# Kernel optimization log

Hardware: AMD Instinct MI355X
Metric: run time of the kernel (lower is better)

Reference implementation:

```python
import jax, jax.numpy as jnp
import numpy as np

DIM = 768
NUM_HEADS = 12
HEAD_DIM = DIM // NUM_HEADS


def setup_inputs() -> dict:
    key = jax.random.key(0)
    k0, k1, k2 = jax.random.split(key, 3)
    B, N = 8, 1024
    x = jax.random.normal(k0, (B, N, DIM), dtype=jnp.float32)
    w_qkv = jax.random.normal(k1, (DIM, 3 * DIM), dtype=jnp.float32) * (DIM ** -0.5)
    b_qkv = jnp.zeros((3 * DIM,), dtype=jnp.float32)
    w_proj = jax.random.normal(k2, (DIM, DIM), dtype=jnp.float32) * (DIM ** -0.5)
    b_proj = jnp.zeros((DIM,), dtype=jnp.float32)
    return {"x": x, "w_qkv": w_qkv, "b_qkv": b_qkv, "w_proj": w_proj, "b_proj": b_proj}


def reference(x, w_qkv, b_qkv, w_proj, b_proj):
    B, N, C = x.shape
    scale = HEAD_DIM ** -0.5
    qkv = x @ w_qkv + b_qkv                                  # [B, N, 3*C]
    qkv = qkv.reshape(B, N, 3, NUM_HEADS, HEAD_DIM).transpose(2, 0, 3, 1, 4)
    q, k, v = qkv[0], qkv[1], qkv[2]                          # each [B, H, N, hd]
    attn = jnp.einsum('bhqd,bhkd->bhqk', q, k) * scale        # [B, H, N, N]
    attn = jax.nn.softmax(attn, axis=-1)
    out = jnp.einsum('bhqk,bhkd->bhqd', attn, v)              # [B, H, N, hd]
    out = out.transpose(0, 2, 1, 3).reshape(B, N, C)
    return out @ w_proj + b_proj
```

## Files before the change

kernel.cpp:

```cpp
#include <hip/hip_runtime.h>
#include <cstdint>
#include <cmath>

#define B_ 8
#define S_ 1024
#define D_ 768
#define H_ 12
#define HD_ 64

typedef __bf16 bf16;
typedef __attribute__((ext_vector_type(8))) __bf16 bf16x8;
typedef __attribute__((ext_vector_type(4))) float floatx4;

typedef const __attribute__((address_space(1))) unsigned int* gas_ptr;
typedef __attribute__((address_space(3))) unsigned int* las_ptr;

__device__ __forceinline__ void async_ld16(const void* g, void* l) {
    gas_ptr gp = (gas_ptr)(uintptr_t)g;
    las_ptr lp = (las_ptr)(unsigned)(uintptr_t)l;
    __builtin_amdgcn_global_load_lds(gp, lp, 16, 0, 0);
}

__device__ __forceinline__ void transpose_dev(const float* __restrict__ in,
                                              bf16* __restrict__ out,
                                              int N, int K, int n0, int k0,
                                              bf16 (*tile)[66], int tid) {
#pragma unroll
    for (int r = 0; r < 4; r++) {
        int idx = r * 256 + tid;
        int row = idx >> 4;
        int c0  = (idx & 15) * 4;
        float4 v = *(const float4*)(in + (size_t)(k0 + row) * N + n0 + c0);
        tile[c0 + 0][row] = (bf16)v.x;
        tile[c0 + 1][row] = (bf16)v.y;
        tile[c0 + 2][row] = (bf16)v.z;
        tile[c0 + 3][row] = (bf16)v.w;
    }
    __syncthreads();
#pragma unroll
    for (int r = 0; r < 2; r++) {
        int idx = r * 256 + tid;
        int orow = idx >> 3;
        int kk   = (idx & 7) * 8;
        union { bf16x8 v; bf16 e[8]; } u;
#pragma unroll
        for (int j = 0; j < 8; j++) u.e[j] = tile[orow][kk + j];
        *(bf16x8*)(out + (size_t)(n0 + orow) * K + k0 + kk) = u.v;
    }
}

__global__ __launch_bounds__(256) void prep_all(
    const float* __restrict__ x, const float* __restrict__ w_qkv,
    const float* __restrict__ w_proj,
    bf16* __restrict__ xb, bf16* __restrict__ wqkvt, bf16* __restrict__ wprojt)
{
    __shared__ bf16 tile[64][66];
    const int blk = blockIdx.x, tid = threadIdx.x;
    if (blk < 6144) {
        int i = (blk * 256 + tid) * 4;
        float4 v = *(const float4*)(x + i);
        xb[i]     = (bf16)v.x;
        xb[i + 1] = (bf16)v.y;
        xb[i + 2] = (bf16)v.z;
        xb[i + 3] = (bf16)v.w;
    } else if (blk < 6576) {
        int t = blk - 6144;
        transpose_dev(w_qkv, wqkvt, 2304, 768, (t % 36) * 64, (t / 36) * 64, tile, tid);
    } else {
        int t = blk - 6576;
        transpose_dev(w_proj, wprojt, 768, 768, (t % 12) * 64, (t / 12) * 64, tile, tid);
    }
}

__global__ void transpose_v(const bf16* __restrict__ vbuf, bf16* __restrict__ vt) {
    __shared__ bf16 tile[64][66];
    const int tid = threadIdx.x;
    const int kt = blockIdx.x, h = blockIdx.y, b = blockIdx.z;
    const bf16* src = vbuf + ((size_t)b * S_ + (size_t)kt * 64) * D_ + h * 64;
#pragma unroll
    for (int r = 0; r < 2; r++) {
        int idx = r * 256 + tid;
        int kr = idx >> 3;
        int d0 = (idx & 7) * 8;
        bf16x8 v = *(const bf16x8*)(src + (size_t)kr * D_ + d0);
#pragma unroll
        for (int j = 0; j < 8; j++) {
            int p  = d0 + j;
            int dt = (p >> 2) + 16 * (p & 3);
            tile[dt][kr] = v[j];
        }
    }
    __syncthreads();
    bf16* dst = vt + ((size_t)(b * H_ + h) * 64) * 1024 + kt * 64;
#pragma unroll
    for (int r = 0; r < 2; r++) {
        int idx = r * 256 + tid;
        int dr = idx >> 3;
        int k0 = (idx & 7) * 8;
        union { bf16x8 v; bf16 e[8]; } u;
#pragma unroll
        for (int j = 0; j < 8; j++) {
            int kp  = k0 + j;
            int grp = kp & 32;
            int w32 = kp & 31;
            int gg  = w32 >> 3;
            int jj  = w32 & 7;
            int tk  = grp + ((jj < 4) ? (4 * gg + jj) : (16 + 4 * gg + jj - 4));
            u.e[j] = tile[dr][tk];
        }
        *(bf16x8*)(dst + (size_t)dr * 1024 + k0) = u.v;
    }
}

__global__ __launch_bounds__(256, 2) void gemm_qkv(
    const bf16* __restrict__ A, const bf16* __restrict__ Bt,
    const float* __restrict__ bias,
    bf16* __restrict__ qpack, bf16* __restrict__ kpack, bf16* __restrict__ vbuf)
{
    __shared__ __align__(16) bf16 As[128 * 32];
    __shared__ __align__(16) bf16 Bs[128 * 32];
    const int N = 2304, K = 768;

    const int tid  = threadIdx.x;
    const int lane = tid & 63;
    const int w    = tid >> 6;
    const int wm   = (w >> 1) * 64;
    const int wn   = (w & 1) * 64;
    const long m0  = (long)blockIdx.y * 128;
    const long n0  = (long)blockIdx.x * 128;
    const int c    = lane & 15;
    const int g    = lane >> 4;

    const floatx4 fzero = {0.f, 0.f, 0.f, 0.f};
    floatx4 acc[4][4];
#pragma unroll
    for (int i = 0; i < 4; i++)
#pragma unroll
        for (int j = 0; j < 4; j++) acc[i][j] = fzero;

    for (int k0 = 0; k0 < K; k0 += 32) {
        __syncthreads();
#pragma unroll
        for (int r = 0; r < 2; r++) {
            const int idx = r * 256 + tid;
            const int row = idx >> 2;
            const int kk  = (idx & 3) * 8;
            async_ld16(A  + (m0 + row) * (long)K + k0 + kk, (char*)As + idx * 16);
            async_ld16(Bt + (n0 + row) * (long)K + k0 + kk, (char*)Bs + idx * 16);
        }
        __syncthreads();

        bf16x8 af[4], bfr[4];
#pragma unroll
        for (int i = 0; i < 4; i++) {
            af[i]  = *(const bf16x8*)(As + (wm + i * 16 + c) * 32 + g * 8);
            bfr[i] = *(const bf16x8*)(Bs + (wn + i * 16 + c) * 32 + g * 8);
        }
#pragma unroll
        for (int i = 0; i < 4; i++)
#pragma unroll
            for (int j = 0; j < 4; j++)
                acc[i][j] = __builtin_amdgcn_mfma_f32_16x16x32_bf16(af[i], bfr[j], acc[i][j], 0, 0, 0);
    }

    const int head = (int)((n0 + wn) >> 6);
    const int rm   = wm + g * 4;
    float bv[4];
#pragma unroll
    for (int j = 0; j < 4; j++) bv[j] = bias[(int)n0 + wn + c + 16 * j];
    const int bb    = (int)(m0 >> 10);
    const int sbase = ((int)m0 & 1023) + rm;

    if (head < 24) {
        const float sc = (head < 12) ? 0.125f : 1.0f;
        bf16* dst = ((head < 12) ? qpack : kpack)
                  + (((size_t)((bb * H_ + (head < 12 ? head : head - 12)) * 1024 + sbase)) << 6)
                  + 4 * c;
#pragma unroll
        for (int i = 0; i < 4; i++)
#pragma unroll
            for (int e = 0; e < 4; e++) {
                union { bf16 h4[4]; uint64_t u; } pk;
#pragma unroll
                for (int j = 0; j < 4; j++) pk.h4[j] = (bf16)((acc[i][j][e] + bv[j]) * sc);
                *(uint64_t*)(dst + (size_t)(i * 16 + e) * 64) = pk.u;
            }
    } else {
        bf16* dst = vbuf + ((size_t)(bb * 1024 + sbase)) * 768 + (head - 24) * 64 + 4 * c;
#pragma unroll
        for (int i = 0; i < 4; i++)
#pragma unroll
            for (int e = 0; e < 4; e++) {
                union { bf16 h4[4]; uint64_t u; } pk;
#pragma unroll
                for (int j = 0; j < 4; j++) pk.h4[j] = (bf16)(acc[i][j][e] + bv[j]);
                *(uint64_t*)(dst + (size_t)(i * 16 + e) * 768) = pk.u;
            }
    }
}

__global__ __launch_bounds__(256, 2) void gemm_bt(
    const bf16* __restrict__ A, const bf16* __restrict__ Bt,
    const float* __restrict__ bias, float* __restrict__ C,
    int M, int N, int K)
{
    __shared__ __align__(16) bf16 As[128 * 32];
    __shared__ __align__(16) bf16 Bs[128 * 32];

    const int tid  = threadIdx.x;
    const int lane = tid & 63;
    const int w    = tid >> 6;
    const int wm   = (w >> 1) * 64;
    const int wn   = (w & 1) * 64;
    const long m0  = (long)blockIdx.y * 128;
    const long n0  = (long)blockIdx.x * 128;
    const int c    = lane & 15;
    const int g    = lane >> 4;

    const floatx4 fzero = {0.f, 0.f, 0.f, 0.f};
    floatx4 acc[4][4];
#pragma unroll
    for (int i = 0; i < 4; i++)
#pragma unroll
        for (int j = 0; j < 4; j++) acc[i][j] = fzero;

    for (int k0 = 0; k0 < K; k0 += 32) {
        __syncthreads();
#pragma unroll
        for (int r = 0; r < 2; r++) {
            const int idx = r * 256 + tid;
            const int row = idx >> 2;
            const int kk  = (idx & 3) * 8;
            async_ld16(A  + (m0 + row) * (long)K + k0 + kk, (char*)As + idx * 16);
            async_ld16(Bt + (n0 + row) * (long)K + k0 + kk, (char*)Bs + idx * 16);
        }
        __syncthreads();

        bf16x8 af[4], bfr[4];
#pragma unroll
        for (int i = 0; i < 4; i++) {
            af[i]  = *(const bf16x8*)(As + (wm + i * 16 + c) * 32 + g * 8);
            bfr[i] = *(const bf16x8*)(Bs + (wn + i * 16 + c) * 32 + g * 8);
        }
#pragma unroll
        for (int i = 0; i < 4; i++)
#pragma unroll
            for (int j = 0; j < 4; j++)
                acc[i][j] = __builtin_amdgcn_mfma_f32_16x16x32_bf16(af[i], bfr[j], acc[i][j], 0, 0, 0);
    }

    const int cn = wn + c;
    const int rm = wm + g * 4;
#pragma unroll
    for (int j = 0; j < 4; j++) {
        const long gn = n0 + cn + j * 16;
        const float bv = bias[gn];
#pragma unroll
        for (int i = 0; i < 4; i++) {
            const long gm = m0 + rm + i * 16;
#pragma unroll
            for (int e = 0; e < 4; e++)
                C[(gm + e) * (long)N + gn] = acc[i][j][e] + bv;
        }
    }
}

__global__ __launch_bounds__(128, 3) void attn_fused(
    const bf16* __restrict__ qpack, const bf16* __restrict__ kpack,
    const bf16* __restrict__ vt, bf16* __restrict__ outp)
{
    __shared__ __align__(16) bf16 Ks[2048];
    __shared__ __align__(16) bf16 Vs[2048];

    const int tid  = threadIdx.x;
    const int lane = tid & 63;
    const int w    = tid >> 6;
    const int g    = lane >> 4;
    const int c    = lane & 15;

    const int id = blockIdx.x;
    const int bh = id % 96;
    const int qt = id / 96;
    const int h  = bh >> 3;
    const int b  = bh & 7;
    const int q0 = qt * 128 + w * 64;
    const bf16* qpb = qpack + ((size_t)(b * H_ + h) * 1024) * 64;
    const bf16* kpb = kpack + ((size_t)(b * H_ + h) * 1024) * 64;
    const bf16* vtb = vt    + ((size_t)(b * H_ + h) * 64) * 1024;

    bf16x8 qf[4][2];
#pragma unroll
    for (int qb = 0; qb < 4; qb++)
#pragma unroll
        for (int dc = 0; dc < 2; dc++)
            qf[qb][dc] = *(const bf16x8*)(qpb + (size_t)(q0 + qb * 16 + c) * 64 + dc * 32 + g * 8);

    union { uint32_t u[4]; bf16x8 v; } onesu;
    onesu.u[0] = onesu.u[1] = onesu.u[2] = onesu.u[3] = 0x3F803F80u;
    const bf16x8 onesf = onesu.v;

    const floatx4 fzero = {0.f, 0.f, 0.f, 0.f};
    floatx4 oacc[4][4];
    floatx4 lacc[4];
#pragma unroll
    for (int qb = 0; qb < 4; qb++) {
        lacc[qb] = fzero;
#pragma unroll
        for (int db = 0; db < 4; db++) oacc[qb][db] = fzero;
    }

    for (int kt = 0; kt < 32; kt++) {
        const int kg = kt * 32;
        __syncthreads();
#pragma unroll
        for (int r = 0; r < 2; r++) {
            const int i  = r * 128 + tid;
            const int dc = i >> 7, key = (i >> 2) & 31, dch = i & 3;
            async_ld16(kpb + (size_t)(kg + key) * 64 + dc * 32 + dch * 8, (char*)Ks + i * 16);
        }
#pragma unroll
        for (int r = 0; r < 2; r++) {
            const int i = r * 128 + tid;
            const int d = i >> 2, kch = i & 3;
            async_ld16(vtb + (size_t)d * 1024 + kg + kch * 8, (char*)Vs + i * 16);
        }
        __syncthreads();

        bf16x8 kf[2][2];
#pragma unroll
        for (int kb = 0; kb < 2; kb++)
#pragma unroll
            for (int dc = 0; dc < 2; dc++)
                kf[kb][dc] = *(const bf16x8*)(Ks + (dc * 32 + kb * 16 + c) * 32 + g * 8);

        bf16x8 vf[4];
#pragma unroll
        for (int db = 0; db < 4; db++)
            vf[db] = *(const bf16x8*)(Vs + (db * 16 + c) * 32 + g * 8);

#pragma unroll
        for (int qb = 0; qb < 4; qb++) {
            floatx4 s0 = fzero, s1 = fzero;
#pragma unroll
            for (int dc = 0; dc < 2; dc++) {
                s0 = __builtin_amdgcn_mfma_f32_16x16x32_bf16(kf[0][dc], qf[qb][dc], s0, 0, 0, 0);
                s1 = __builtin_amdgcn_mfma_f32_16x16x32_bf16(kf[1][dc], qf[qb][dc], s1, 0, 0, 0);
            }
            union { bf16 e[8]; bf16x8 v; } pa;
#pragma unroll
            for (int e4 = 0; e4 < 4; e4++) {
                pa.e[e4]     = (bf16)__expf(s0[e4]);
                pa.e[e4 + 4] = (bf16)__expf(s1[e4]);
            }
            lacc[qb] = __builtin_amdgcn_mfma_f32_16x16x32_bf16(onesf, pa.v, lacc[qb], 0, 0, 0);
#pragma unroll
            for (int db = 0; db < 4; db++)
                oacc[qb][db] = __builtin_amdgcn_mfma_f32_16x16x32_bf16(vf[db], pa.v, oacc[qb][db], 0, 0, 0);
        }
    }

#pragma unroll
    for (int qb = 0; qb < 4; qb++) {
        const float linv = 1.0f / lacc[qb][0];
        bf16* orow = outp + ((size_t)b * S_ + q0 + qb * 16 + c) * D_ + h * 64;
#pragma unroll
        for (int db = 0; db < 4; db++)
#pragma unroll
            for (int f = 0; f < 2; f++) {
                union { bf16 hh[2]; uint32_t u; } pk_;
                pk_.hh[0] = (bf16)(oacc[qb][db][2 * f]     * linv);
                pk_.hh[1] = (bf16)(oacc[qb][db][2 * f + 1] * linv);
                *(uint32_t*)(orow + db * 16 + 4 * g + 2 * f) = pk_.u;
            }
    }
}

extern "C" void kernel_launch(void* const* d_in, const int* in_sizes, int n_in,
                              void* d_out, int out_size, void* d_ws, size_t ws_size,
                              hipStream_t stream) {
    const float* x      = (const float*)d_in[0];
    const float* w_qkv  = (const float*)d_in[1];
    const float* b_qkv  = (const float*)d_in[2];
    const float* w_proj = (const float*)d_in[3];
    const float* b_proj = (const float*)d_in[4];
    float* out = (float*)d_out;

    bf16* xb     = (bf16*)d_ws;
    bf16* wqkvt  = xb     + (size_t)8192 * 768;
    bf16* wprojt = wqkvt  + (size_t)2304 * 768;
    bf16* qpack  = wprojt + (size_t)768 * 768;
    bf16* kpack  = qpack  + (size_t)96 * 1024 * 64;
    bf16* vbuf   = kpack  + (size_t)96 * 1024 * 64;
    bf16* vt     = vbuf   + (size_t)8192 * 768;
    bf16* attnb  = xb;

    prep_all<<<6720, 256, 0, stream>>>(x, w_qkv, w_proj, xb, wqkvt, wprojt);
    gemm_qkv<<<dim3(18, 64), 256, 0, stream>>>(xb, wqkvt, b_qkv, qpack, kpack, vbuf);
    transpose_v<<<dim3(16, 12, 8), 256, 0, stream>>>(vbuf, vt);
    attn_fused<<<768, 128, 0, stream>>>(qpack, kpack, vt, attnb);
    gemm_bt<<<dim3(6, 64), 256, 0, stream>>>(attnb, wprojt, b_proj, out, 8192, 768, 768);
}
```

Baseline: 202.9 us.

## Double-buffer K/V tiles in LDS to overlap async loads with compute

Attention K and V tiles now live in two LDS buffers. The next tile's async global-to-LDS loads are issued before computing on the current one, and inline s_waitcnt vmcnt/s_barrier replaces the two __syncthreads per iteration. A second barrier after the fragment reads keeps the buffer from being overwritten while still in use. The aim is to hide global load latency behind MFMA work, at the cost of doubled LDS use (possibly lower occupancy) and hand-written waitcnt sequencing that relies on the exact count of outstanding loads.

```diff
diff --git a/kernel.cpp b/kernel.cpp
--- a/kernel.cpp
+++ b/kernel.cpp
@@ -269,8 +269,8 @@
     const bf16* __restrict__ qpack, const bf16* __restrict__ kpack,
     const bf16* __restrict__ vt, bf16* __restrict__ outp)
 {
-    __shared__ __align__(16) bf16 Ks[2048];
-    __shared__ __align__(16) bf16 Vs[2048];
+    __shared__ __align__(16) bf16 Ks[2][2048];
+    __shared__ __align__(16) bf16 Vs[2][2048];
 
     const int tid  = threadIdx.x;
     const int lane = tid & 63;
@@ -288,6 +288,22 @@
     const bf16* kpb = kpack + ((size_t)(b * H_ + h) * 1024) * 64;
     const bf16* vtb = vt    + ((size_t)(b * H_ + h) * 64) * 1024;
 
+    auto stage = [&](int kt_, bf16* Kbuf, bf16* Vbuf) {
+        const int kg = kt_ * 32;
+#pragma unroll
+        for (int r = 0; r < 2; r++) {
+            const int i  = r * 128 + tid;
+            const int dc = i >> 7, key = (i >> 2) & 31, dch = i & 3;
+            async_ld16(kpb + (size_t)(kg + key) * 64 + dc * 32 + dch * 8, (char*)Kbuf + i * 16);
+        }
+#pragma unroll
+        for (int r = 0; r < 2; r++) {
+            const int i = r * 128 + tid;
+            const int d = i >> 2, kch = i & 3;
+            async_ld16(vtb + (size_t)d * 1024 + kg + kch * 8, (char*)Vbuf + i * 16);
+        }
+    };
+
     bf16x8 qf[4][2];
 #pragma unroll
     for (int qb = 0; qb < 4; qb++)
@@ -309,34 +325,33 @@
         for (int db = 0; db < 4; db++) oacc[qb][db] = fzero;
     }
 
+    stage(0, Ks[0], Vs[0]);
+
+#pragma unroll 2
     for (int kt = 0; kt < 32; kt++) {
-        const int kg = kt * 32;
-        __syncthreads();
-#pragma unroll
-        for (int r = 0; r < 2; r++) {
-            const int i  = r * 128 + tid;
-            const int dc = i >> 7, key = (i >> 2) & 31, dch = i & 3;
-            async_ld16(kpb + (size_t)(kg + key) * 64 + dc * 32 + dch * 8, (char*)Ks + i * 16);
-        }
-#pragma unroll
-        for (int r = 0; r < 2; r++) {
-            const int i = r * 128 + tid;
-            const int d = i >> 2, kch = i & 3;
-            async_ld16(vtb + (size_t)d * 1024 + kg + kch * 8, (char*)Vs + i * 16);
-        }
-        __syncthreads();
+        const int cur = kt & 1;
+        bf16* Kc = Ks[cur];
+        bf16* Vc = Vs[cur];
+        if (kt < 31) {
+            stage(kt + 1, Ks[cur ^ 1], Vs[cur ^ 1]);
+            asm volatile("s_waitcnt vmcnt(4)\n\ts_barrier" ::: "memory");
+        } else {
+            asm volatile("s_waitcnt vmcnt(0)\n\ts_barrier" ::: "memory");
+        }
 
         bf16x8 kf[2][2];
 #pragma unroll
         for (int kb = 0; kb < 2; kb++)
 #pragma unroll
             for (int dc = 0; dc < 2; dc++)
-                kf[kb][dc] = *(const bf16x8*)(Ks + (dc * 32 + kb * 16 + c) * 32 + g * 8);
+                kf[kb][dc] = *(const bf16x8*)(Kc + (dc * 32 + kb * 16 + c) * 32 + g * 8);
 
         bf16x8 vf[4];
 #pragma unroll
         for (int db = 0; db < 4; db++)
-            vf[db] = *(const bf16x8*)(Vs + (db * 16 + c) * 32 + g * 8);
+            vf[db] = *(const bf16x8*)(Vc + (db * 16 + c) * 32 + g * 8);
+
+        asm volatile("s_waitcnt lgkmcnt(0)\n\ts_barrier" ::: "memory");
 
 #pragma unroll
         for (int qb = 0; qb < 4; qb++) {
```

Result: slower. 230.9 us (+13.8%).
